# Kernel tuning notes

Measured on AMD Instinct MI355X. Metric: run time of the kernel, lower is better.

## Reference

```python
import jax, jax.numpy as jnp
import numpy as np

N = 50000      # nodes
E = 1600000    # edges (nnz of A)
D_IN = 512
D_H = 512
D_OUT = 40
L = 3
LN_EPS = 1e-5
BN_EPS = 1e-5


def setup_inputs() -> dict:
    key = jax.random.key(0)
    ks = jax.random.split(key, 10)
    x = jax.random.normal(ks[0], (N, D_IN), dtype=jnp.float32)
    edge_src = jax.random.randint(ks[1], (E,), 0, N, dtype=jnp.int32)
    edge_dst = jax.random.randint(ks[2], (E,), 0, N, dtype=jnp.int32)
    s = 1.0 / np.sqrt(D_IN)
    W_in = (jax.random.normal(ks[3], (D_IN, D_H), dtype=jnp.float32) * s)
    b_in = jnp.zeros((D_H,), jnp.float32)
    ln_g = jnp.ones((D_H,), jnp.float32)
    ln_b = jnp.zeros((D_H,), jnp.float32)
    cW1 = (jax.random.normal(ks[4], (D_H, D_H), dtype=jnp.float32) * s)
    cb1 = jnp.zeros((D_H,), jnp.float32)
    bn_g = 1.0 + 0.1 * jax.random.normal(ks[5], (D_H,), dtype=jnp.float32)
    bn_b = 0.1 * jax.random.normal(ks[6], (D_H,), dtype=jnp.float32)
    bn_mean = jnp.zeros((D_H,), jnp.float32)   # eval-mode running stats
    bn_var = jnp.ones((D_H,), jnp.float32)
    cW2 = (jax.random.normal(ks[7], (D_H, D_OUT), dtype=jnp.float32) * s)
    cb2 = jnp.zeros((D_OUT,), jnp.float32)
    return dict(x=x, edge_src=edge_src, edge_dst=edge_dst, W_in=W_in, b_in=b_in,
                ln_g=ln_g, ln_b=ln_b, cW1=cW1, cb1=cb1, bn_g=bn_g, bn_b=bn_b,
                bn_mean=bn_mean, bn_var=bn_var, cW2=cW2, cb2=cb2)


def _agg_angle(h, edge_src, edge_dst, dinv):
    # diag(D^-1/2 A D^-1/2 @ CosSim^T)[i] = sum_{(i,j) in A} dinv_i dinv_j cos(h_i,h_j)
    nrm = jnp.sqrt(jnp.sum(h * h, axis=1, keepdims=True))  # torch.norm p=2
    hn = h / (nrm + 1e-4)
    cos_e = jnp.clip(jnp.sum(hn[edge_src] * hn[edge_dst], axis=1), -1.0, 1.0)  # [E]
    w_e = dinv[edge_src] * dinv[edge_dst] * cos_e
    return jax.ops.segment_sum(w_e, edge_src, num_segments=N)  # [N]


def _forward(x, edge_src, edge_dst, W_in, b_in, ln_g, ln_b, cW1, cb1,
             bn_g, bn_b, bn_mean, bn_var, cW2, cb2):
    h = jax.nn.relu(x @ W_in + b_in)
    mu = jnp.mean(h, axis=-1, keepdims=True)
    var = jnp.var(h, axis=-1, keepdims=True)
    h = (h - mu) / jnp.sqrt(var + LN_EPS) * ln_g + ln_b   # LayerNorm
    # dropout: eval mode -> identity
    # degree normalization (adjacency values are all 1.0); constant across layers
    deg = jax.ops.segment_sum(jnp.ones((E,), h.dtype), edge_src, num_segments=N)
    dinv = jnp.where(deg > 0, deg ** -0.5, 0.0)
    for _ in range(L):
        ang = _agg_angle(h, edge_src, edge_dst, dinv)  # [N]
        c, s = jnp.cos(ang), jnp.sin(ang)
        r0 = c * h[:, 0] - s * h[:, 1]   # 2x2 Givens rotation on first two dims
        r1 = s * h[:, 0] + c * h[:, 1]
        h = jnp.concatenate([jnp.stack([r0, r1], axis=1), h[:, 2:]], axis=1)
    # classifier: Linear -> ReLU -> BatchNorm1d (eval) -> Linear
    z = jax.nn.relu(h @ cW1 + cb1)
    z = (z - bn_mean) / jnp.sqrt(bn_var + BN_EPS) * bn_g + bn_b
    logits = z @ cW2 + cb2
    return jax.nn.log_softmax(logits, axis=1)


def reference(x, edge_src, edge_dst, W_in, b_in, ln_g, ln_b, cW1, cb1,
              bn_g, bn_b, bn_mean, bn_var, cW2, cb2):
    return _forward(x, edge_src, edge_dst, W_in, b_in, ln_g, ln_b, cW1, cb1,
                    bn_g, bn_b, bn_mean, bn_var, cW2, cb2)
```

## Files before the change

kernel.cpp:

```cpp
#include <hip/hip_runtime.h>
#include <hip/hip_bf16.h>
#include <math.h>

typedef unsigned short u16;
typedef unsigned int u32;

#define N_NODES 50000
#define N_EDGES 1600000
#define DIM     512
#define DOUT    40
#define MPAD    50048
#define QROW    256
#define NBKT    196
#define NB1     256
#define CHUNK   6250

typedef __bf16 bf16x8 __attribute__((ext_vector_type(8)));
typedef float  f32x4  __attribute__((ext_vector_type(4)));

__device__ inline u16 f2bf(float f) {
    union { float f; u32 u; } v; v.f = f;
    u32 u = v.u;
    u32 r = u + 0x7fffu + ((u >> 16) & 1u);
    return (u16)(r >> 16);
}
__device__ inline float2 bfpair(u32 u) {
    float2 r;
    union { u32 i; float f; } lo, hi;
    lo.i = u << 16; hi.i = u & 0xffff0000u;
    r.x = lo.f; r.y = hi.f; return r;
}
__device__ inline float wave_sum(float v) {
    #pragma unroll
    for (int o = 32; o > 0; o >>= 1) v += __shfl_xor(v, o);
    return v;
}
__device__ inline float wave_max(float v) {
    #pragma unroll
    for (int o = 32; o > 0; o >>= 1) v = fmaxf(v, __shfl_xor(v, o));
    return v;
}
__device__ inline int wave_sum_i(int v) {
    #pragma unroll
    for (int o = 32; o > 0; o >>= 1) v += __shfl_xor(v, o);
    return v;
}
#if __has_builtin(__builtin_amdgcn_sdot8)
__device__ inline int dot8(int a, int b, int c) {
    return __builtin_amdgcn_sdot8(a, b, c, false);
}
#else
__device__ inline int dot8(int a, int b, int c) {
    #pragma unroll
    for (int j = 0; j < 8; ++j) {
        int av = ((int)((u32)a << (28 - 4 * j))) >> 28;
        int bv = ((int)((u32)b << (28 - 4 * j))) >> 28;
        c += av * bv;
    }
    return c;
}
#endif
__device__ inline void gload16(const void* g, void* l) {
    __builtin_amdgcn_global_load_lds((const __attribute__((address_space(1))) u32*)g,
                                     (__attribute__((address_space(3))) u32*)l, 16, 0, 0);
}
__device__ inline int block_incl_scan(int v, int tid) {
    int lane = tid & 63, w = tid >> 6;
    #pragma unroll
    for (int o = 1; o < 64; o <<= 1) {
        int t = __shfl_up(v, o);
        if (lane >= o) v += t;
    }
    __shared__ int wsum[4];
    if (lane == 63) wsum[w] = v;
    __syncthreads();
    if (w > 0) v += wsum[0];
    if (w > 1) v += wsum[1];
    if (w > 2) v += wsum[2];
    return v;
}

__global__ __launch_bounds__(256) void k_conv_x(const float* __restrict__ x,
                                                u16* __restrict__ xb) {
    long idx = (long)blockIdx.x * 256 + threadIdx.x;
    long base = idx * 4;
    if (base >= (long)MPAD * DIM) return;
    long row = base >> 9;
    float4 v;
    if (row < N_NODES) v = *(const float4*)(x + base);
    else { v.x = v.y = v.z = v.w = 0.f; }
    ushort4 o;
    o.x = f2bf(v.x); o.y = f2bf(v.y); o.z = f2bf(v.z); o.w = f2bf(v.w);
    *(ushort4*)(xb + base) = o;
}

__global__ __launch_bounds__(256) void k_prep(const float* __restrict__ W_in,
                                              const float* __restrict__ cW1,
                                              const float* __restrict__ cW2,
                                              u16* __restrict__ WtIn,
                                              u16* __restrict__ W1t,
                                              u16* __restrict__ W2b) {
    int z = blockIdx.z;
    if (z < 2) {
        const float* W = z ? cW1 : W_in;
        u16* T = z ? W1t : WtIn;
        int n = blockIdx.x * 16 + threadIdx.x;
        int k = blockIdx.y * 16 + threadIdx.y;
        T[(long)n * 512 + k] = f2bf(W[(long)k * 512 + n]);
    } else {
        int idx = (blockIdx.y * 32 + blockIdx.x) * 256 + threadIdx.y * 16 + threadIdx.x;
        if (idx < 48 * DIM) {
            int n = idx >> 9;
            int k = idx & 511;
            float v = (n < DOUT) ? cW2[(long)k * DOUT + n] : 0.f;
            W2b[idx] = f2bf(v);
        }
    }
}

__global__ __launch_bounds__(256) void k_ms_count(const int* __restrict__ esrc,
                                                  int* __restrict__ C) {
    __shared__ int bcnt[NBKT];
    int tid = threadIdx.x, blk = blockIdx.x;
    if (tid < NBKT) bcnt[tid] = 0;
    __syncthreads();
    int e0 = blk * CHUNK, e1 = e0 + CHUNK;
    for (int e = e0 + tid; e < e1; e += 256)
        atomicAdd(&bcnt[esrc[e] >> 8], 1);
    __syncthreads();
    if (tid < NBKT) C[tid * NB1 + blk] = bcnt[tid];
}
__global__ __launch_bounds__(256) void k_ms_scan_partial(const int* __restrict__ C,
                                                         int* __restrict__ psum2) {
    int v = C[blockIdx.x * 256 + threadIdx.x];
    int t = wave_sum_i(v);
    __shared__ int ws[4];
    int lane = threadIdx.x & 63, w = threadIdx.x >> 6;
    if (lane == 0) ws[w] = t;
    __syncthreads();
    if (threadIdx.x == 0) psum2[blockIdx.x] = ws[0] + ws[1] + ws[2] + ws[3];
}
__global__ __launch_bounds__(256) void k_ms_scan_base(const int* __restrict__ psum2,
                                                      int* __restrict__ pb2) {
    int tid = threadIdx.x;
    int v = (tid < NBKT) ? psum2[tid] : 0;
    int incl = block_incl_scan(v, tid);
    if (tid < NBKT) pb2[tid] = incl - v;
}
__global__ __launch_bounds__(256) void k_ms_scan_add(const int* __restrict__ C,
                                                     const int* __restrict__ pb2,
                                                     int* __restrict__ O) {
    int idx = blockIdx.x * 256 + threadIdx.x;
    int v = C[idx];
    int incl = block_incl_scan(v, threadIdx.x);
    O[idx] = pb2[blockIdx.x] + incl - v;
}
__global__ __launch_bounds__(256) void k_ms_scatter(const int* __restrict__ esrc,
                                                    const int* __restrict__ edst,
                                                    const int* __restrict__ O,
                                                    u32* __restrict__ pk) {
    __shared__ int cur[NBKT];
    int tid = threadIdx.x, blk = blockIdx.x;
    if (tid < NBKT) cur[tid] = O[tid * NB1 + blk];
    __syncthreads();
    int e0 = blk * CHUNK, e1 = e0 + CHUNK;
    for (int e = e0 + tid; e < e1; e += 256) {
        int s = esrc[e], d = edst[e];
        int pos = atomicAdd(&cur[s >> 8], 1);
        pk[pos] = ((u32)(s & 255) << 16) | (u32)d;
    }
}
__global__ __launch_bounds__(256) void k_bucket(const int* __restrict__ Om,
                                                const u32* __restrict__ pk,
                                                int* __restrict__ rowptr,
                                                float* __restrict__ dinv,
                                                u16* __restrict__ edst_s) {
    __shared__ int cnt[256];
    __shared__ int curs[256];
    int tid = threadIdx.x, b = blockIdx.x;
    int base = b * 256;
    int start = Om[b * NB1];
    int end = (b == NBKT - 1) ? N_EDGES : Om[(b + 1) * NB1];
    cnt[tid] = 0;
    __syncthreads();
    for (int p = start + tid; p < end; p += 256)
        atomicAdd(&cnt[pk[p] >> 16], 1);
    __syncthreads();
    int c = cnt[tid];
    int incl = block_incl_scan(c, tid);
    int excl = incl - c;
    int node = base + tid;
    if (node < N_NODES) {
        rowptr[node] = start + excl;
        dinv[node] = (c > 0) ? (1.f / sqrtf((float)c)) : 0.f;
    }
    if (b == NBKT - 1 && tid == 0) rowptr[N_NODES] = N_EDGES;
    curs[tid] = start + excl;
    __syncthreads();
    for (int p = start + tid; p < end; p += 256) {
        u32 pr = pk[p];
        int pos = atomicAdd(&curs[pr >> 16], 1);
        edst_s[pos] = (u16)(pr & 0xFFFFu);
    }
}

template<int EPI>
__global__ __launch_bounds__(256) void k_gemm(const u16* __restrict__ A,
                                              const u16* __restrict__ Bt,
                                              u16* __restrict__ outB,
                                              const float* __restrict__ bias,
                                              const float* __restrict__ bn_g,
                                              const float* __restrict__ bn_b,
                                              const float* __restrict__ bn_mean,
                                              const float* __restrict__ bn_var) {
    __shared__ u16 lds[2 * 128 * 64];
    char* ldsA = (char*)lds;
    char* ldsB = (char*)lds + 16384;

    const int bid = blockIdx.x;
    const int xcd = bid & 7;
    const int j = bid >> 3;
    const int tm = xcd * 49 + (j >> 2);
    const int tn = j & 3;
    if (tm >= MPAD / 128) return;

    const int tid = threadIdx.x;
    const int l = tid & 63, wid = tid >> 6;
    const int wr = wid >> 1, wc = wid & 1;
    const int lm = l & 15, lk = l >> 4;

    const int srow = tid >> 3;
    const int kq   = tid & 7;

    f32x4 acc[4][4] = {};

    for (int kt = 0; kt < 8; ++kt) {
        const int k0 = kt * 64;
        #pragma unroll
        for (int r = 0; r < 4; ++r) {
            int row = r * 32 + srow;
            int kc = (kq ^ (row & 7)) * 8;
            const u16* ga = A + ((long)tm * 128 + row) * DIM + k0 + kc;
            const u16* gb = Bt + ((long)tn * 128 + row) * DIM + k0 + kc;
            char* la = ldsA + r * 4096 + wid * 1024;
            char* lb = ldsB + r * 4096 + wid * 1024;
            gload16(ga, la);
            gload16(gb, lb);
        }
        __syncthreads();
        #pragma unroll
        for (int kk = 0; kk < 2; ++kk) {
            bf16x8 af[4], bfr[4];
            #pragma unroll
            for (int m = 0; m < 4; ++m) {
                int ar = wr * 64 + m * 16 + lm;
                af[m] = *(const bf16x8*)(ldsA + ar * 128 + ((kk * 64 + lk * 16) ^ ((ar & 7) << 4)));
            }
            #pragma unroll
            for (int n = 0; n < 4; ++n) {
                int br = wc * 64 + n * 16 + lm;
                bfr[n] = *(const bf16x8*)(ldsB + br * 128 + ((kk * 64 + lk * 16) ^ ((br & 7) << 4)));
            }
            #pragma unroll
            for (int m = 0; m < 4; ++m)
                #pragma unroll
                for (int n = 0; n < 4; ++n)
                    acc[m][n] = __builtin_amdgcn_mfma_f32_16x16x32_bf16(af[m], bfr[n], acc[m][n], 0, 0, 0);
        }
        __syncthreads();
    }

    #pragma unroll
    for (int n = 0; n < 4; ++n) {
        int col = tn * 128 + wc * 64 + n * 16 + lm;
        float bc = bias[col];
        float scale = 0.f, shift = 0.f;
        if (EPI == 1) {
            scale = bn_g[col] / sqrtf(bn_var[col] + 1e-5f);
            shift = bn_b[col] - bn_mean[col] * scale;
        }
        #pragma unroll
        for (int m = 0; m < 4; ++m) {
            f32x4 v = acc[m][n];
            #pragma unroll
            for (int r = 0; r < 4; ++r) {
                long row = (long)tm * 128 + wr * 64 + m * 16 + lk * 4 + r;
                float val = fmaxf(v[r] + bc, 0.f);
                if (EPI == 1) val = val * scale + shift;
                outB[row * DIM + col] = f2bf(val);
            }
        }
    }
}

__global__ __launch_bounds__(256) void k_ln(u16* __restrict__ hb,
                                            char* __restrict__ hq,
                                            const float* __restrict__ dinv,
                                            const float* __restrict__ g,
                                            const float* __restrict__ b,
                                            float* __restrict__ a0,
                                            float* __restrict__ a1,
                                            float* __restrict__ inv_nrm,
                                            float4* __restrict__ nd) {
    int row = blockIdx.x * 4 + (threadIdx.x >> 6);
    int l = threadIdx.x & 63;
    u16* prow = hb + (long)row * DIM + l * 8;
    if (row >= N_NODES) {
        if (row < MPAD) { uint4 z; z.x = z.y = z.z = z.w = 0u; *(uint4*)prow = z; }
        return;
    }
    uint4 v = *(const uint4*)prow;
    float x[8];
    { float2 p;
      p = bfpair(v.x); x[0] = p.x; x[1] = p.y;
      p = bfpair(v.y); x[2] = p.x; x[3] = p.y;
      p = bfpair(v.z); x[4] = p.x; x[5] = p.y;
      p = bfpair(v.w); x[6] = p.x; x[7] = p.y; }
    float s = 0.f, sq = 0.f;
    #pragma unroll
    for (int j = 0; j < 8; ++j) { s += x[j]; sq += x[j] * x[j]; }
    #pragma unroll
    for (int o = 32; o > 0; o >>= 1) { s += __shfl_xor(s, o); sq += __shfl_xor(sq, o); }
    float mean = s * (1.f / DIM);
    float var = sq * (1.f / DIM) - mean * mean;
    float rstd = 1.f / sqrtf(var + 1e-5f);
    float y[8];
    #pragma unroll
    for (int j = 0; j < 8; ++j) {
        int c = l * 8 + j;
        y[j] = (x[j] - mean) * rstd * g[c] + b[c];
    }
    float s2 = 0.f;
    #pragma unroll
    for (int j = 0; j < 8; ++j) s2 += y[j] * y[j];
    s2 = wave_sum(s2);
    float nrm = sqrtf(s2);
    float inv = 1.f / (nrm + 1e-4f);
    ushort4 oh;
    oh.x = f2bf(y[0]); oh.y = f2bf(y[1]); oh.z = f2bf(y[2]); oh.w = f2bf(y[3]);
    *(ushort4*)prow = oh;
    oh.x = f2bf(y[4]); oh.y = f2bf(y[5]); oh.z = f2bf(y[6]); oh.w = f2bf(y[7]);
    *(ushort4*)(prow + 4) = oh;
    float nv[8];
    float mx = 0.f;
    #pragma unroll
    for (int j = 0; j < 8; ++j) { nv[j] = y[j] * inv; mx = fmaxf(mx, fabsf(nv[j])); }
    mx = wave_max(mx);
    float qs = (mx > 0.f) ? (7.f / mx) : 0.f;
    if (l == 0) { nv[0] = 0.f; nv[1] = 0.f; }
    u32 w = 0;
    #pragma unroll
    for (int j = 0; j < 8; ++j) {
        int q = (int)rintf(nv[j] * qs);
        w |= ((u32)(q & 0xF)) << (4 * j);
    }
    *(u32*)(hq + (long)row * QROW + l * 4) = w;
    if (l == 0) {
        float st = (mx > 0.f) ? (mx * (1.f / 7.f)) : 0.f;
        a0[row] = y[0]; a1[row] = y[1]; inv_nrm[row] = inv;
        float4 n4; n4.x = y[0] * inv; n4.y = y[1] * inv; n4.z = dinv[row]; n4.w = st;
        nd[row] = n4;
    }
}

__global__ __launch_bounds__(256) void k_edge_dot(const int* __restrict__ rowptr,
                                                  const u16* __restrict__ edst_s,
                                                  const char* __restrict__ hq,
                                                  const float4* __restrict__ ndI,
                                                  const float* __restrict__ a0i,
                                                  const float* __restrict__ a1i,
                                                  const float* __restrict__ invn,
                                                  float* __restrict__ rest,
                                                  float* __restrict__ a0o,
                                                  float* __restrict__ a1o,
                                                  float4* __restrict__ ndO) {
    int node = blockIdx.x * 4 + (threadIdx.x >> 6);
    if (node >= N_NODES) return;
    int l = threadIdx.x & 63;
    int le = l & 7;
    int eg = l >> 3;
    int p0 = rowptr[node], p1 = rowptr[node + 1];
    float4 own = ndI[node];
    float xa = a0i[node], ya = a1i[node];
    if (p0 == p1) {
        if (l == 0) { a0o[node] = xa; a1o[node] = ya; ndO[node] = own; }
        return;
    }
    const int4* srow = (const int4*)(hq + (long)node * QROW);
    int4 s0 = srow[le * 2], s1 = srow[le * 2 + 1];
    float ss = own.w;
    float sa0 = own.x, sa1 = own.y;
    float accum = 0.f;
    #pragma unroll 4
    for (int base = p0; base < p1; base += 8) {
        int p = base + eg;
        bool ok = p < p1;
        int d = ok ? (int)edst_s[p] : 0;
        const int4* drow = (const int4*)(hq + (long)d * QROW);
        int4 d0 = drow[le * 2], d1 = drow[le * 2 + 1];
        int acc = 0;
        acc = dot8(s0.x, d0.x, acc); acc = dot8(s0.y, d0.y, acc);
        acc = dot8(s0.z, d0.z, acc); acc = dot8(s0.w, d0.w, acc);
        acc = dot8(s1.x, d1.x, acc); acc = dot8(s1.y, d1.y, acc);
        acc = dot8(s1.z, d1.z, acc); acc = dot8(s1.w, d1.w, acc);
        acc += __shfl_xor(acc, 4);
        acc += __shfl_xor(acc, 2);
        acc += __shfl_xor(acc, 1);
        if (ok && le == 0) {
            float4 ndd = ndI[d];
            float r = ss * ndd.w * (float)acc;
            rest[p] = r;
            float c = r + sa0 * ndd.x + sa1 * ndd.y;
            c = fminf(1.f, fmaxf(-1.f, c));
            accum += ndd.z * c;
        }
    }
    accum = wave_sum(accum);
    if (l == 0) {
        float ang = own.z * accum;
        float sn, cs;
        sincosf(ang, &sn, &cs);
        float r0 = cs * xa - sn * ya;
        float r1 = sn * xa + cs * ya;
        a0o[node] = r0;
        a1o[node] = r1;
        float inv = invn[node];
        float4 n4; n4.x = r0 * inv; n4.y = r1 * inv; n4.z = own.z; n4.w = own.w;
        ndO[node] = n4;
    }
}

template<int WRITE_HB>
__global__ __launch_bounds__(256) void k_layer(const int* __restrict__ rowptr,
                                               const u16* __restrict__ edst_s,
                                               const float* __restrict__ rest,
                                               const float4* __restrict__ ndI,
                                               const float* __restrict__ a0i,
                                               const float* __restrict__ a1i,
                                               const float* __restrict__ invn,
                                               float* __restrict__ a0o,
                                               float* __restrict__ a1o,
                                               float4* __restrict__ ndO,
                                               u16* __restrict__ hb) {
    int node = blockIdx.x * 4 + (threadIdx.x >> 6);
    if (node >= N_NODES) return;
    int l = threadIdx.x & 63;
    int p0 = rowptr[node], p1 = rowptr[node + 1];
    float4 own = ndI[node];
    float x = a0i[node], y = a1i[node];
    float sa0 = own.x, sa1 = own.y;
    float accum = 0.f;
    for (int p = p0 + l; p < p1; p += 64) {
        int d = (int)edst_s[p];
        float4 ndd = ndI[d];
        float c = rest[p] + sa0 * ndd.x + sa1 * ndd.y;
        c = fminf(1.f, fmaxf(-1.f, c));
        accum += ndd.z * c;
    }
    accum = wave_sum(accum);
    if (l == 0) {
        float ang = own.z * accum;
        float sn, cs;
        sincosf(ang, &sn, &cs);
        float r0 = cs * x - sn * y;
        float r1 = sn * x + cs * y;
        if (WRITE_HB) {
            hb[(long)node * DIM + 0] = f2bf(r0);
            hb[(long)node * DIM + 1] = f2bf(r1);
        } else {
            a0o[node] = r0;
            a1o[node] = r1;
            float inv = invn[node];
            float4 n4; n4.x = r0 * inv; n4.y = r1 * inv; n4.z = own.z; n4.w = own.w;
            ndO[node] = n4;
        }
    }
}

__global__ __launch_bounds__(256) void k_final(const u16* __restrict__ zb,
                                               const u16* __restrict__ W2b,
                                               const float* __restrict__ cb2,
                                               float* __restrict__ out) {
    __shared__ char ldsB[48 * 1024];
    const int tid = threadIdx.x;
    #pragma unroll
    for (int i = 0; i < 12; ++i) {
        int unit = i * 256 + tid;
        int byte = unit * 16;
        int row = byte >> 10;
        int colb = byte & 1023;
        uint4 v = *(const uint4*)((const char*)W2b + byte);
        *(uint4*)(ldsB + row * 1024 + (colb ^ ((row & 7) << 4))) = v;
    }
    __syncthreads();

    const int l = tid & 63, wid = tid >> 6;
    const int lm = l & 15, lk = l >> 4;
    const long m0 = (long)blockIdx.x * 128 + wid * 32;

    f32x4 acc[2][3] = {};
    for (int kt = 0; kt < 16; ++kt) {
        const int k0 = kt * 32;
        bf16x8 af[2], bfr[3];
        #pragma unroll
        for (int m = 0; m < 2; ++m)
            af[m] = *(const bf16x8*)(zb + (m0 + m * 16 + lm) * DIM + k0 + lk * 8);
        #pragma unroll
        for (int n = 0; n < 3; ++n) {
            int br = n * 16 + lm;
            bfr[n] = *(const bf16x8*)(ldsB + br * 1024 + ((k0 * 2 + lk * 16) ^ ((br & 7) << 4)));
        }
        #pragma unroll
        for (int m = 0; m < 2; ++m)
            #pragma unroll
            for (int n = 0; n < 3; ++n)
                acc[m][n] = __builtin_amdgcn_mfma_f32_16x16x32_bf16(af[m], bfr[n], acc[m][n], 0, 0, 0);
    }

    float bc[3];
    #pragma unroll
    for (int n = 0; n < 3; ++n) {
        int col = n * 16 + lm;
        bc[n] = (col < DOUT) ? cb2[col] : 0.f;
    }

    #pragma unroll
    for (int m = 0; m < 2; ++m) {
        #pragma unroll
        for (int r = 0; r < 4; ++r) {
            long row = m0 + m * 16 + lk * 4 + r;
            float v[3];
            float mv = -1e30f;
            #pragma unroll
            for (int n = 0; n < 3; ++n) {
                int col = n * 16 + lm;
                float t = (col < DOUT) ? (acc[m][n][r] + bc[n]) : -1e30f;
                v[n] = t;
                mv = fmaxf(mv, t);
            }
            #pragma unroll
            for (int o = 8; o > 0; o >>= 1) mv = fmaxf(mv, __shfl_xor(mv, o));
            float es = 0.f;
            #pragma unroll
            for (int n = 0; n < 3; ++n) {
                int col = n * 16 + lm;
                if (col < DOUT) es += expf(v[n] - mv);
            }
            #pragma unroll
            for (int o = 8; o > 0; o >>= 1) es += __shfl_xor(es, o);
            float lse = logf(es);
            if (row < N_NODES) {
                #pragma unroll
                for (int n = 0; n < 3; ++n) {
                    int col = n * 16 + lm;
                    if (col < DOUT) out[row * DOUT + col] = v[n] - mv - lse;
                }
            }
        }
    }
}

extern "C" void kernel_launch(void* const* d_in, const int* in_sizes, int n_in,
                              void* d_out, int out_size, void* d_ws, size_t ws_size,
                              hipStream_t stream) {
    const float* x       = (const float*)d_in[0];
    const int*   esrc    = (const int*)d_in[1];
    const int*   edst    = (const int*)d_in[2];
    const float* W_in    = (const float*)d_in[3];
    const float* b_in    = (const float*)d_in[4];
    const float* ln_g    = (const float*)d_in[5];
    const float* ln_b    = (const float*)d_in[6];
    const float* cW1     = (const float*)d_in[7];
    const float* cb1     = (const float*)d_in[8];
    const float* bn_g    = (const float*)d_in[9];
    const float* bn_b    = (const float*)d_in[10];
    const float* bn_mean = (const float*)d_in[11];
    const float* bn_var  = (const float*)d_in[12];
    const float* cW2     = (const float*)d_in[13];
    const float* cb2     = (const float*)d_in[14];
    float* out = (float*)d_out;

    char* ws = (char*)d_ws;
    size_t off = 0;
    auto take = [&](size_t bytes) -> char* {
        char* p = ws + off;
        off = (off + bytes + 255) & ~(size_t)255;
        return p;
    };
    u16*    xb     = (u16*)take((size_t)MPAD * DIM * 2);
    u16*    hb     = (u16*)take((size_t)MPAD * DIM * 2);
    char*   hq     = (char*)take((size_t)N_NODES * QROW);
    u16*    WtIn   = (u16*)take((size_t)512 * 512 * 2);
    u16*    W1t    = (u16*)take((size_t)512 * 512 * 2);
    u16*    W2b    = (u16*)take((size_t)48 * 512 * 2);
    float*  dinv   = (float*)take((size_t)N_NODES * 4);
    float*  a0A    = (float*)take((size_t)N_NODES * 4);
    float*  a1A    = (float*)take((size_t)N_NODES * 4);
    float*  a0B    = (float*)take((size_t)N_NODES * 4);
    float*  a1B    = (float*)take((size_t)N_NODES * 4);
    float*  invn   = (float*)take((size_t)N_NODES * 4);
    float4* ndA    = (float4*)take((size_t)N_NODES * 16);
    float4* ndB    = (float4*)take((size_t)N_NODES * 16);
    float*  rest   = (float*)take((size_t)N_EDGES * 4);
    int*    rowptr = (int*)take((size_t)(N_NODES + 1) * 4);
    u16*    edst_s = (u16*)take((size_t)N_EDGES * 2);
    u32*    pk     = (u32*)take((size_t)N_EDGES * 4);
    int*    Cm     = (int*)take((size_t)NBKT * NB1 * 4);
    int*    Om     = (int*)take((size_t)NBKT * NB1 * 4);
    int*    psum2  = (int*)take((size_t)NBKT * 4);
    int*    pb2    = (int*)take((size_t)NBKT * 4);
    u16*    zb     = xb;

    k_conv_x<<<(MPAD * DIM / 4 + 255) / 256, 256, 0, stream>>>(x, xb);
    k_prep<<<dim3(32, 32, 3), dim3(16, 16), 0, stream>>>(W_in, cW1, cW2, WtIn, W1t, W2b);

    k_ms_count<<<NB1, 256, 0, stream>>>(esrc, Cm);
    k_ms_scan_partial<<<NBKT, 256, 0, stream>>>(Cm, psum2);
    k_ms_scan_base<<<1, 256, 0, stream>>>(psum2, pb2);
    k_ms_scan_add<<<NBKT, 256, 0, stream>>>(Cm, pb2, Om);
    k_ms_scatter<<<NB1, 256, 0, stream>>>(esrc, edst, Om, pk);
    k_bucket<<<NBKT, 256, 0, stream>>>(Om, pk, rowptr, dinv, edst_s);

    k_gemm<0><<<1568, 256, 0, stream>>>(xb, WtIn, hb, b_in,
                                        nullptr, nullptr, nullptr, nullptr);
    k_ln<<<MPAD / 4, 256, 0, stream>>>(hb, hq, dinv, ln_g, ln_b, a0A, a1A, invn, ndA);
    k_edge_dot<<<(N_NODES + 3) / 4, 256, 0, stream>>>(rowptr, edst_s, hq, ndA,
                                                      a0A, a1A, invn, rest, a0B, a1B, ndB);
    k_layer<0><<<(N_NODES + 3) / 4, 256, 0, stream>>>(rowptr, edst_s, rest, ndB,
                                                      a0B, a1B, invn, a0A, a1A, ndA, nullptr);
    k_layer<1><<<(N_NODES + 3) / 4, 256, 0, stream>>>(rowptr, edst_s, rest, ndA,
                                                      a0A, a1A, invn, nullptr, nullptr, nullptr, hb);

    k_gemm<1><<<1568, 256, 0, stream>>>(hb, W1t, zb, cb1,
                                        bn_g, bn_b, bn_mean, bn_var);
    k_final<<<MPAD / 128, 256, 0, stream>>>(zb, W2b, cb2, out);
}
```

Measured before the change: 307.7 us.

## Merge conversion/prep kernels, vectorize edge sort loads, store residual dots in bf16

Three changes land together. The x-to-bf16 conversion and weight preparation kernels become one launch, which removes a kernel boundary. The bucket-count and scatter passes now read source and destination indices as int4, which requires changing the chunk size so that it divides by four (NB1 becomes 250 and CHUNK 6400). The per-edge residual cosine term is stored as bf16 instead of fp32, halving its traffic across the layer passes at the cost of some precision in the cosine sums.

```diff
diff --git a/kernel.cpp b/kernel.cpp
--- a/kernel.cpp
+++ b/kernel.cpp
@@ -12,8 +12,8 @@
 #define MPAD    50048
 #define QROW    256
 #define NBKT    196
-#define NB1     256
-#define CHUNK   6250
+#define NB1     250
+#define CHUNK   6400
 
 typedef __bf16 bf16x8 __attribute__((ext_vector_type(8)));
 typedef float  f32x4  __attribute__((ext_vector_type(4)));
@@ -24,6 +24,9 @@
     u32 r = u + 0x7fffu + ((u >> 16) & 1u);
     return (u16)(r >> 16);
 }
+__device__ inline float bf2f(u16 u) {
+    union { u32 i; float f; } v; v.i = ((u32)u) << 16; return v.f;
+}
 __device__ inline float2 bfpair(u32 u) {
     float2 r;
     union { u32 i; float f; } lo, hi;
@@ -80,35 +83,37 @@
     return v;
 }
 
-__global__ __launch_bounds__(256) void k_conv_x(const float* __restrict__ x,
-                                                u16* __restrict__ xb) {
-    long idx = (long)blockIdx.x * 256 + threadIdx.x;
-    long base = idx * 4;
-    if (base >= (long)MPAD * DIM) return;
-    long row = base >> 9;
-    float4 v;
-    if (row < N_NODES) v = *(const float4*)(x + base);
-    else { v.x = v.y = v.z = v.w = 0.f; }
-    ushort4 o;
-    o.x = f2bf(v.x); o.y = f2bf(v.y); o.z = f2bf(v.z); o.w = f2bf(v.w);
-    *(ushort4*)(xb + base) = o;
-}
-
-__global__ __launch_bounds__(256) void k_prep(const float* __restrict__ W_in,
+#define CONV_BLKS 25024
+__global__ __launch_bounds__(256) void k_prep(const float* __restrict__ x,
+                                              u16* __restrict__ xb,
+                                              const float* __restrict__ W_in,
                                               const float* __restrict__ cW1,
                                               const float* __restrict__ cW2,
                                               u16* __restrict__ WtIn,
                                               u16* __restrict__ W1t,
                                               u16* __restrict__ W2b) {
-    int z = blockIdx.z;
-    if (z < 2) {
+    int b = blockIdx.x, tid = threadIdx.x;
+    if (b < CONV_BLKS) {
+        long idx = (long)b * 256 + tid;
+        long base = idx * 4;
+        long row = base >> 9;
+        float4 v;
+        if (row < N_NODES) v = *(const float4*)(x + base);
+        else { v.x = v.y = v.z = v.w = 0.f; }
+        ushort4 o;
+        o.x = f2bf(v.x); o.y = f2bf(v.y); o.z = f2bf(v.z); o.w = f2bf(v.w);
+        *(ushort4*)(xb + base) = o;
+    } else if (b < CONV_BLKS + 2048) {
+        int t = b - CONV_BLKS;
+        int z = t >> 10;
+        int q = t & 1023;
         const float* W = z ? cW1 : W_in;
         u16* T = z ? W1t : WtIn;
-        int n = blockIdx.x * 16 + threadIdx.x;
-        int k = blockIdx.y * 16 + threadIdx.y;
+        int n = (q & 31) * 16 + (tid & 15);
+        int k = (q >> 5) * 16 + (tid >> 4);
         T[(long)n * 512 + k] = f2bf(W[(long)k * 512 + n]);
     } else {
-        int idx = (blockIdx.y * 32 + blockIdx.x) * 256 + threadIdx.y * 16 + threadIdx.x;
+        int idx = (b - CONV_BLKS - 2048) * 256 + tid;
         if (idx < 48 * DIM) {
             int n = idx >> 9;
             int k = idx & 511;
@@ -124,15 +129,21 @@
     int tid = threadIdx.x, blk = blockIdx.x;
     if (tid < NBKT) bcnt[tid] = 0;
     __syncthreads();
-    int e0 = blk * CHUNK, e1 = e0 + CHUNK;
-    for (int e = e0 + tid; e < e1; e += 256)
-        atomicAdd(&bcnt[esrc[e] >> 8], 1);
+    const int4* e4 = (const int4*)(esrc + blk * CHUNK);
+    for (int i = tid; i < CHUNK / 4; i += 256) {
+        int4 v = e4[i];
+        atomicAdd(&bcnt[v.x >> 8], 1);
+        atomicAdd(&bcnt[v.y >> 8], 1);
+        atomicAdd(&bcnt[v.z >> 8], 1);
+        atomicAdd(&bcnt[v.w >> 8], 1);
+    }
     __syncthreads();
     if (tid < NBKT) C[tid * NB1 + blk] = bcnt[tid];
 }
 __global__ __launch_bounds__(256) void k_ms_scan_partial(const int* __restrict__ C,
                                                          int* __restrict__ psum2) {
-    int v = C[blockIdx.x * 256 + threadIdx.x];
+    int idx = blockIdx.x * NB1 + threadIdx.x;
+    int v = (threadIdx.x < NB1) ? C[idx] : 0;
     int t = wave_sum_i(v);
     __shared__ int ws[4];
     int lane = threadIdx.x & 63, w = threadIdx.x >> 6;
@@ -150,10 +161,10 @@
 __global__ __launch_bounds__(256) void k_ms_scan_add(const int* __restrict__ C,
                                                      const int* __restrict__ pb2,
                                                      int* __restrict__ O) {
-    int idx = blockIdx.x * 256 + threadIdx.x;
-    int v = C[idx];
-    int incl = block_incl_scan(v, threadIdx.x);
-    O[idx] = pb2[blockIdx.x] + incl - v;
+    int tid = threadIdx.x;
+    int v = (tid < NB1) ? C[blockIdx.x * NB1 + tid] : 0;
+    int incl = block_incl_scan(v, tid);
+    if (tid < NB1) O[blockIdx.x * NB1 + tid] = pb2[blockIdx.x] + incl - v;
 }
 __global__ __launch_bounds__(256) void k_ms_scatter(const int* __restrict__ esrc,
                                                     const int* __restrict__ edst,
@@ -163,11 +174,15 @@
     int tid = threadIdx.x, blk = blockIdx.x;
     if (tid < NBKT) cur[tid] = O[tid * NB1 + blk];
     __syncthreads();
-    int e0 = blk * CHUNK, e1 = e0 + CHUNK;
-    for (int e = e0 + tid; e < e1; e += 256) {
-        int s = esrc[e], d = edst[e];
-        int pos = atomicAdd(&cur[s >> 8], 1);
-        pk[pos] = ((u32)(s & 255) << 16) | (u32)d;
+    const int4* s4 = (const int4*)(esrc + blk * CHUNK);
+    const int4* d4 = (const int4*)(edst + blk * CHUNK);
+    for (int i = tid; i < CHUNK / 4; i += 256) {
+        int4 s = s4[i], d = d4[i];
+        int pos;
+        pos = atomicAdd(&cur[s.x >> 8], 1); pk[pos] = ((u32)(s.x & 255) << 16) | (u32)d.x;
+        pos = atomicAdd(&cur[s.y >> 8], 1); pk[pos] = ((u32)(s.y & 255) << 16) | (u32)d.y;
+        pos = atomicAdd(&cur[s.z >> 8], 1); pk[pos] = ((u32)(s.z & 255) << 16) | (u32)d.z;
+        pos = atomicAdd(&cur[s.w >> 8], 1); pk[pos] = ((u32)(s.w & 255) << 16) | (u32)d.w;
     }
 }
 __global__ __launch_bounds__(256) void k_bucket(const int* __restrict__ Om,
@@ -370,7 +385,7 @@
                                                   const float* __restrict__ a0i,
                                                   const float* __restrict__ a1i,
                                                   const float* __restrict__ invn,
-                                                  float* __restrict__ rest,
+                                                  u16* __restrict__ rest,
                                                   float* __restrict__ a0o,
                                                   float* __restrict__ a1o,
                                                   float4* __restrict__ ndO) {
@@ -409,7 +424,7 @@
         if (ok && le == 0) {
             float4 ndd = ndI[d];
             float r = ss * ndd.w * (float)acc;
-            rest[p] = r;
+            rest[p] = f2bf(r);
             float c = r + sa0 * ndd.x + sa1 * ndd.y;
             c = fminf(1.f, fmaxf(-1.f, c));
             accum += ndd.z * c;
@@ -433,7 +448,7 @@
 template<int WRITE_HB>
 __global__ __launch_bounds__(256) void k_layer(const int* __restrict__ rowptr,
                                                const u16* __restrict__ edst_s,
-                                               const float* __restrict__ rest,
+                                               const u16* __restrict__ rest,
                                                const float4* __restrict__ ndI,
                                                const float* __restrict__ a0i,
                                                const float* __restrict__ a1i,
@@ -453,7 +468,7 @@
     for (int p = p0 + l; p < p1; p += 64) {
         int d = (int)edst_s[p];
         float4 ndd = ndI[d];
-        float c = rest[p] + sa0 * ndd.x + sa1 * ndd.y;
+        float c = bf2f(rest[p]) + sa0 * ndd.x + sa1 * ndd.y;
         c = fminf(1.f, fmaxf(-1.f, c));
         accum += ndd.z * c;
     }
@@ -601,7 +616,7 @@
     float*  invn   = (float*)take((size_t)N_NODES * 4);
     float4* ndA    = (float4*)take((size_t)N_NODES * 16);
     float4* ndB    = (float4*)take((size_t)N_NODES * 16);
-    float*  rest   = (float*)take((size_t)N_EDGES * 4);
+    u16*    rest   = (u16*)take((size_t)N_EDGES * 2);
     int*    rowptr = (int*)take((size_t)(N_NODES + 1) * 4);
     u16*    edst_s = (u16*)take((size_t)N_EDGES * 2);
     u32*    pk     = (u32*)take((size_t)N_EDGES * 4);
@@ -611,8 +626,8 @@
     int*    pb2    = (int*)take((size_t)NBKT * 4);
     u16*    zb     = xb;
 
-    k_conv_x<<<(MPAD * DIM / 4 + 255) / 256, 256, 0, stream>>>(x, xb);
-    k_prep<<<dim3(32, 32, 3), dim3(16, 16), 0, stream>>>(W_in, cW1, cW2, WtIn, W1t, W2b);
+    k_prep<<<CONV_BLKS + 2048 + 96, 256, 0, stream>>>(x, xb, W_in, cW1, cW2,
+                                                      WtIn, W1t, W2b);
 
     k_ms_count<<<NB1, 256, 0, stream>>>(esrc, Cm);
     k_ms_scan_partial<<<NBKT, 256, 0, stream>>>(Cm, psum2);
```

New measurement: 293.6 us. 1.05x faster.
